# Optimization experiments

Measured on AMD Instinct MI355X. Metric: run time of the kernel, lower is better.

The kernel has to match this reference:

```python
import jax, jax.numpy as jnp
import numpy as np
from jax import lax

V, E, T, F, K = 100000, 300, 50, 100, 3
B, S = 32, 512


def setup_inputs() -> dict:
    key = jax.random.key(0)
    ks = jax.random.split(key, 10)
    inp = {
        "x": jax.random.randint(ks[0], (B, S), 0, V),
        "tags": jax.random.randint(ks[1], (B, S), 0, T),
        "emb": jax.random.normal(ks[2], (V, E), dtype=jnp.float32),
        "conv_w": jax.random.normal(ks[3], (F, E, K), dtype=jnp.float32) / np.sqrt(E * K),
        "conv_b": jnp.zeros((F,), dtype=jnp.float32),
        "fc_w": jax.random.normal(ks[4], (T, F), dtype=jnp.float32) / np.sqrt(F),
        "fc_b": jnp.zeros((T,), dtype=jnp.float32),
        "start_trans": jax.random.uniform(ks[5], (T,), dtype=jnp.float32, minval=-0.1, maxval=0.1),
        "end_trans": jax.random.uniform(ks[6], (T,), dtype=jnp.float32, minval=-0.1, maxval=0.1),
        "trans": jax.random.uniform(ks[7], (T, T), dtype=jnp.float32, minval=-0.1, maxval=0.1),
    }
    return inp


def _emissions(x, emb, conv_w, conv_b, fc_w, fc_b):
    e = emb[x]                                   # [B,S,E] embedding gather
    e = jnp.transpose(e, (0, 2, 1))              # [B,E,S]
    h = lax.conv_general_dilated(e, conv_w, (1,), [(K // 2, K // 2)])  # [B,F,S] (NCW/OIW)
    h = jax.nn.relu(h + conv_b[None, :, None])   # dropout is identity in eval
    feat = jnp.transpose(h, (0, 2, 1))           # [B,S,F]
    return (jnp.einsum("bsf,tf->bst", feat, fc_w) + fc_b).astype(jnp.float32)  # [B,S,T]


def _crf_nll(emissions, tags, start_trans, end_trans, trans):
    # numerator: score of the gold tag path (full mask)
    em_tag = jnp.take_along_axis(emissions, tags[..., None], axis=-1)[..., 0]  # [B,S]
    num = (start_trans[tags[:, 0]]
           + em_tag.sum(-1)
           + trans[tags[:, :-1], tags[:, 1:]].sum(-1)
           + end_trans[tags[:, -1]])                                           # [B]

    # denominator: forward algorithm via scan over time
    alpha0 = start_trans[None, :] + emissions[:, 0]                             # [B,T]

    def step(alpha, em_t):
        # alpha: [B,T] prev scores; em_t: [B,T] emissions at t
        new = jax.nn.logsumexp(alpha[:, :, None] + trans[None] + em_t[:, None, :], axis=1)
        return new, None

    alpha, _ = lax.scan(step, alpha0, jnp.transpose(emissions[:, 1:], (1, 0, 2)))
    log_z = jax.nn.logsumexp(alpha + end_trans[None, :], axis=-1)               # [B]
    return -(num - log_z).sum()  # torchcrf default reduction='sum'; model returns -llh


def reference(x, tags, emb, conv_w, conv_b, fc_w, fc_b, start_trans, end_trans, trans):
    emissions = _emissions(x, emb, conv_w, conv_b, fc_w, fc_b)
    return _crf_nll(emissions, tags, start_trans, end_trans, trans)
```

## Files before the change

### kernel.cpp

```cpp
#include <hip/hip_runtime.h>
#include <hip/hip_bf16.h>
#include <math.h>

#define BB 32
#define SS 512
#define EE 300
#define FF 100
#define TT 50
#define CH 16
#define NC 32

typedef __attribute__((ext_vector_type(8))) short v8s;
typedef __attribute__((ext_vector_type(4))) float v4f;
#define MFMA16 __builtin_amdgcn_mfma_f32_16x16x32_bf16

#define AP 328
#define NCH 10
#define CKS 3
#define CHB (128 * 96)
#define A2P 136
#define MP 72

__device__ inline unsigned short f2bf(float v) {
    unsigned u = __float_as_uint(v);
    unsigned r = u + 0x7fff + ((u >> 16) & 1);
    return (unsigned short)(r >> 16);
}
__device__ inline float bf2f(short s) {
    return __uint_as_float(((unsigned)(unsigned short)s) << 16);
}
__device__ inline unsigned pkbf2(float a, float b) {
    __hip_bfloat162 h = __float22bfloat162_rn(make_float2(a, b));
    return *(unsigned*)&h;
}
__device__ inline v8s ldsld8(const short* p) {
    return *(const v8s*)__builtin_assume_aligned(p, 16);
}
__device__ inline void g2lds16(const void* g, void* l) {
    __builtin_amdgcn_global_load_lds(
        (const __attribute__((address_space(1))) unsigned int*)g,
        (__attribute__((address_space(3))) unsigned int*)l, 16, 0, 0);
}

__global__ void prep_kernel(const float* __restrict__ tr, const float* __restrict__ cw,
                            const float* __restrict__ fcw,
                            unsigned short* __restrict__ wB2,
                            unsigned short* __restrict__ fcwT2,
                            unsigned short* __restrict__ AT,
                            unsigned short* __restrict__ Ab,
                            float* __restrict__ accum, unsigned* __restrict__ cnt)
{
    const int gid = blockIdx.x * 256 + threadIdx.x;
    const int gs  = 64 * 256;
    if (gid == 0) { *accum = 0.f; *cnt = 0u; }
    for (int idx = gid; idx < NCH * CKS * 8 * 512; idx += gs) {
        int e = idx & 7, p = (idx >> 3) & 63, blk = idx >> 9;
        int ch = blk / 24, rem = blk - ch * 24;
        int sl = rem >> 3, ft = rem & 7;
        int col = p >> 2, q = p & 3;
        int n  = ft * 16 + col;
        int gk = ch * 96 + sl * 32 + q * 8 + e;
        int kk = gk / 320, ee = gk - kk * 320;
        float v = (n < FF && ee < EE) ? cw[n * 900 + ee * 3 + kk] : 0.f;
        wB2[idx] = f2bf(v);
    }
    for (int idx = gid; idx < 16 * 512; idx += gs) {
        int e = idx & 7, p = (idx >> 3) & 63, blk = idx >> 9;
        int ks = blk >> 2, nt = blk & 3;
        int col = p >> 2, q = p & 3;
        int t = nt * 16 + col, f = ks * 32 + q * 8 + e;
        float v = (t < TT && f < FF) ? fcw[t * FF + f] : 0.f;
        fcwT2[idx] = f2bf(v);
    }
    for (int idx = gid; idx < 64 * 64; idx += gs) {
        int r = idx >> 6, c2 = idx & 63;
        AT[idx] = (r < TT && c2 < TT) ? f2bf(__expf(tr[c2 * TT + r])) : 0;
        Ab[idx] = (r < TT && c2 < TT) ? f2bf(__expf(tr[r * TT + c2])) : 0;
    }
}

__global__ __launch_bounds__(256, 2) void emis_kernel(
    const int* __restrict__ x, const float* __restrict__ emb,
    const unsigned short* __restrict__ wB2, const float* __restrict__ cb,
    const unsigned short* __restrict__ fcwT2, const float* __restrict__ fcb,
    const int* __restrict__ tags,
    float* __restrict__ expem, float* __restrict__ rmv, float* __restrict__ emtag)
{
    __shared__ __align__(16) short ldsA[34 * AP];
    __shared__ __align__(16) short ldsB[2 * CHB];

    const int b    = blockIdx.y;
    const int s0   = blockIdx.x * 32;
    const int tid  = threadIdx.x;
    const int wv   = tid >> 6;
    const int lane = tid & 63;
    const int col  = lane & 15;
    const int q    = lane >> 4;
    const int bofs = ((col << 2) | q) << 3;

#pragma unroll
    for (int it = 0; it < 6; ++it) {
        int seg = it * 4 + wv;
        g2lds16((const char*)wB2 + seg * 1024 + lane * 16,
                (char*)ldsB + seg * 1024);
    }

    int   xr[10], ofs[10], e0a[10];
#pragma unroll
    for (int it = 0; it < 10; ++it) {
        int g = tid + it * 256;
        int r = g / 75, eg = g - r * 75;
        int e0 = eg * 4;
        int src = s0 - 1 + r;
        bool v = (g < 2550) && (src >= 0) && (src < SS);
        xr[it]  = v ? x[b * SS + src] : -1;
        ofs[it] = r * AP + e0;
        e0a[it] = e0;
    }
    float4 vv[10];
#pragma unroll
    for (int it = 0; it < 10; ++it)
        vv[it] = (xr[it] >= 0)
               ? *(const float4*)(emb + (size_t)xr[it] * EE + e0a[it])
               : make_float4(0.f, 0.f, 0.f, 0.f);
#pragma unroll
    for (int it = 0; it < 10; ++it) {
        int g = tid + it * 256;
        if (g < 2550) {
            unsigned lo = pkbf2(vv[it].x, vv[it].y);
            unsigned hi = pkbf2(vv[it].z, vv[it].w);
            *(uint2*)&ldsA[ofs[it]] = make_uint2(lo, hi);
        }
    }
    if (tid < 34 * 5) {
        int r = tid / 5, c0 = 300 + (tid % 5) * 4;
        *(short4*)&ldsA[r * AP + c0] = make_short4(0, 0, 0, 0);
    }

    v4f acc[2][2];
#pragma unroll
    for (int a = 0; a < 2; ++a)
#pragma unroll
        for (int f = 0; f < 2; ++f) acc[a][f] = (v4f){0.f, 0.f, 0.f, 0.f};

    const int ftA = wv * 2, ftB = wv * 2 + 1;
    for (int ch = 0; ch < NCH; ++ch) {
        __syncthreads();
        if (ch < NCH - 1) {
            const char* g = (const char*)(wB2 + (size_t)(ch + 1) * CHB);
            char* l = (char*)ldsB + ((ch + 1) & 1) * (CHB * 2);
#pragma unroll
            for (int it = 0; it < 6; ++it) {
                int seg = it * 4 + wv;
                g2lds16(g + seg * 1024 + lane * 16, l + seg * 1024);
            }
        } else {
#pragma unroll
            for (int it = 0; it < 4; ++it) {
                int seg = it * 4 + wv;
                g2lds16((const char*)fcwT2 + seg * 1024 + lane * 16,
                        (char*)ldsB + seg * 1024);
            }
        }
        const short* Bc = ldsB + (ch & 1) * CHB;
#pragma unroll
        for (int sl = 0; sl < CKS; ++sl) {
            int gk = ch * 96 + sl * 32;
            int kk = (gk >= 640) ? 2 : (gk >= 320 ? 1 : 0);
            int e0 = gk - kk * 320;
            v8s a0 = ldsld8(&ldsA[(col + kk) * AP + e0 + q * 8]);
            v8s a1 = ldsld8(&ldsA[(16 + col + kk) * AP + e0 + q * 8]);
            v8s b0 = ldsld8(&Bc[((sl * 8 + ftA) << 9) + bofs]);
            v8s b1 = ldsld8(&Bc[((sl * 8 + ftB) << 9) + bofs]);
            acc[0][0] = MFMA16(a0, b0, acc[0][0], 0, 0, 0);
            acc[0][1] = MFMA16(a0, b1, acc[0][1], 0, 0, 0);
            acc[1][0] = MFMA16(a1, b0, acc[1][0], 0, 0, 0);
            acc[1][1] = MFMA16(a1, b1, acc[1][1], 0, 0, 0);
        }
    }
    __syncthreads();

    short* A2 = ldsA;
    short* B2 = ldsB;
#pragma unroll
    for (int st = 0; st < 2; ++st)
#pragma unroll
        for (int fi = 0; fi < 2; ++fi) {
            int f = (wv * 2 + fi) * 16 + col;
            float bias = (f < FF) ? cb[f] : 0.f;
#pragma unroll
            for (int rg = 0; rg < 4; ++rg) {
                int s = st * 16 + q * 4 + rg;
                float v = (f < FF) ? fmaxf(acc[st][fi][rg] + bias, 0.f) : 0.f;
                A2[s * A2P + f] = (short)f2bf(v);
            }
        }
    __syncthreads();

    if (wv < 2) {
        v4f a2[4];
#pragma unroll
        for (int nt = 0; nt < 4; ++nt) a2[nt] = (v4f){0.f, 0.f, 0.f, 0.f};
#pragma unroll
        for (int ks = 0; ks < 4; ++ks) {
            v8s af = ldsld8(&A2[(wv * 16 + col) * A2P + ks * 32 + q * 8]);
#pragma unroll
            for (int nt = 0; nt < 4; ++nt) {
                v8s bt = ldsld8(&B2[((ks * 4 + nt) << 9) + bofs]);
                a2[nt] = MFMA16(af, bt, a2[nt], 0, 0, 0);
            }
        }
        float fb0 = fcb[col], fb1 = fcb[16 + col], fb2 = fcb[32 + col];
        float fb3 = (col < 2) ? fcb[48 + col] : 0.f;
#pragma unroll
        for (int rg = 0; rg < 4; ++rg) {
            int s = s0 + wv * 16 + q * 4 + rg;
            float e0v = a2[0][rg] + fb0;
            float e1v = a2[1][rg] + fb1;
            float e2v = a2[2][rg] + fb2;
            float e3v = (col < 2) ? a2[3][rg] + fb3 : -1e30f;
            float m = fmaxf(fmaxf(e0v, e1v), fmaxf(e2v, e3v));
#pragma unroll
            for (int off = 1; off < 16; off <<= 1) m = fmaxf(m, __shfl_xor(m, off));
            int gidx = b * SS + s;
            if (col == 0) rmv[gidx] = m;
            int tg = tags[gidx];
            float* orow = expem + (size_t)gidx * TT;
            orow[col]      = __expf(e0v - m);
            orow[16 + col] = __expf(e1v - m);
            orow[32 + col] = __expf(e2v - m);
            if (col < 2) orow[48 + col] = __expf(e3v - m);
            if (tg == col)            emtag[gidx] = e0v;
            else if (tg == 16 + col)  emtag[gidx] = e1v;
            else if (tg == 32 + col)  emtag[gidx] = e2v;
            else if (col < 2 && tg == 48 + col) emtag[gidx] = e3v;
        }
    }
}

__global__ __launch_bounds__(64) void chunk_kernel(
    const float* __restrict__ expem, const unsigned short* __restrict__ AT,
    const unsigned short* __restrict__ Ab,
    unsigned short* __restrict__ R, float* __restrict__ lsR)
{
    __shared__ __align__(16) short L[2][64 * MP];
    __shared__ __align__(16) float emL[CH][64];
    const int c = blockIdx.x, b = blockIdx.y;
    const int lane = threadIdx.x;
    const int col = lane & 15, q = lane >> 4;
    const int t0 = c * CH + 1;
    const int nf = (c == NC - 1) ? (SS - 1 - (NC - 1) * CH) : CH;

    for (int idx = lane; idx < CH * 64; idx += 64) {
        int k = idx >> 6, m = idx & 63;
        float v = 0.f;
        if (m < TT && k < nf) v = expem[((size_t)(b * SS + t0 + k)) * TT + m];
        emL[k][m] = v;
    }

    v8s af[4][2];
#pragma unroll
    for (int jt = 0; jt < 4; ++jt)
#pragma unroll
        for (int kc = 0; kc < 2; ++kc)
            af[jt][kc] = *(const v8s*)(AT + (jt * 16 + col) * 64 + kc * 32 + q * 8);
    __syncthreads();

    {
        const v8s* arow = (const v8s*)(Ab + lane * 64);
#pragma unroll
        for (int g = 0; g < 8; ++g) {
            v8s a = arow[g];
            float f[8];
#pragma unroll
            for (int e = 0; e < 8; ++e) f[e] = bf2f(a[e]) * emL[0][g * 8 + e];
            uint4 o = make_uint4(pkbf2(f[0], f[1]), pkbf2(f[2], f[3]),
                                 pkbf2(f[4], f[5]), pkbf2(f[6], f[7]));
            *(uint4*)&L[0][lane * MP + g * 8] = o;
        }
    }

    int cur = 0;
    for (int k = 1; k < nf; ++k) {
        __syncthreads();
        v8s bf[4][2];
#pragma unroll
        for (int nt = 0; nt < 4; ++nt)
#pragma unroll
            for (int kc = 0; kc < 2; ++kc)
                bf[nt][kc] = ldsld8(&L[cur][(nt * 16 + col) * MP + kc * 32 + q * 8]);
        v4f acc[4][4];
#pragma unroll
        for (int jt = 0; jt < 4; ++jt)
#pragma unroll
            for (int nt = 0; nt < 4; ++nt) {
                acc[jt][nt] = (v4f){0.f, 0.f, 0.f, 0.f};
                acc[jt][nt] = MFMA16(af[jt][0], bf[nt][0], acc[jt][nt], 0, 0, 0);
                acc[jt][nt] = MFMA16(af[jt][1], bf[nt][1], acc[jt][nt], 0, 0, 0);
            }
        if (k < nf - 1) {
#pragma unroll
            for (int jt = 0; jt < 4; ++jt) {
                const float4 em4 = *(const float4*)&emL[k][jt * 16 + q * 4];
#pragma unroll
                for (int nt = 0; nt < 4; ++nt) {
                    uint2 o = make_uint2(
                        pkbf2(acc[jt][nt][0] * em4.x, acc[jt][nt][1] * em4.y),
                        pkbf2(acc[jt][nt][2] * em4.z, acc[jt][nt][3] * em4.w));
                    *(uint2*)&L[cur ^ 1][(nt * 16 + col) * MP + jt * 16 + q * 4] = o;
                }
            }
            cur ^= 1;
        } else {
            float vals[4][4][4];
            float mx = 0.f;
#pragma unroll
            for (int jt = 0; jt < 4; ++jt) {
                const float4 em4 = *(const float4*)&emL[k][jt * 16 + q * 4];
#pragma unroll
                for (int nt = 0; nt < 4; ++nt) {
                    vals[jt][nt][0] = acc[jt][nt][0] * em4.x;
                    vals[jt][nt][1] = acc[jt][nt][1] * em4.y;
                    vals[jt][nt][2] = acc[jt][nt][2] * em4.z;
                    vals[jt][nt][3] = acc[jt][nt][3] * em4.w;
#pragma unroll
                    for (int r = 0; r < 4; ++r) mx = fmaxf(mx, vals[jt][nt][r]);
                }
            }
#pragma unroll
            for (int off = 1; off < 64; off <<= 1) mx = fmaxf(mx, __shfl_xor(mx, off));
            mx = fmaxf(mx, 1e-37f);
            float inv = 1.f / mx;
            unsigned short* Rc = R + ((size_t)(b * NC + c) << 12);
#pragma unroll
            for (int jt = 0; jt < 4; ++jt)
#pragma unroll
                for (int nt = 0; nt < 4; ++nt)
#pragma unroll
                    for (int r = 0; r < 4; ++r)
                        Rc[(jt * 16 + q * 4 + r) * 64 + nt * 16 + col] =
                            f2bf(vals[jt][nt][r] * inv);
            if (lane == 0) lsR[b * NC + c] = __logf(mx);
        }
    }
}

__device__ inline float chaindot(const v8s (&buf)[8], const float* pvec) {
    const float4* pv4 = (const float4*)__builtin_assume_aligned(pvec, 16);
    float a0 = 0.f, a1 = 0.f, a2 = 0.f, a3 = 0.f;
#pragma unroll
    for (int g = 0; g < 8; ++g) {
        v8s v = buf[g];
        float4 pA = pv4[g * 2], pB = pv4[g * 2 + 1];
        float* aa = (g & 3) == 0 ? &a0 : (g & 3) == 1 ? &a1 : (g & 3) == 2 ? &a2 : &a3;
        float t = *aa;
        t = fmaf(bf2f(v[0]), pA.x, t);
        t = fmaf(bf2f(v[1]), pA.y, t);
        t = fmaf(bf2f(v[2]), pA.z, t);
        t = fmaf(bf2f(v[3]), pA.w, t);
        t = fmaf(bf2f(v[4]), pB.x, t);
        t = fmaf(bf2f(v[5]), pB.y, t);
        t = fmaf(bf2f(v[6]), pB.z, t);
        t = fmaf(bf2f(v[7]), pB.w, t);
        *aa = t;
    }
    return (a0 + a1) + (a2 + a3);
}

__device__ inline void chainfin(float acc2, float* pvec, int i, float& logacc) {
    float mx = acc2;
#pragma unroll
    for (int off = 1; off < 64; off <<= 1) mx = fmaxf(mx, __shfl_xor(mx, off));
    mx = fmaxf(mx, 1e-37f);
    logacc += __logf(mx);
    pvec[i] = acc2 * (1.f / mx);
}

__global__ __launch_bounds__(256) void chain_kernel(
    const float* __restrict__ expem, const unsigned short* __restrict__ R,
    const float* __restrict__ lsR, const float* __restrict__ start,
    const float* __restrict__ endt,
    const float* __restrict__ emtag, const float* __restrict__ rmv,
    const int* __restrict__ tags, const float* __restrict__ tr,
    float* __restrict__ accum, unsigned* __restrict__ cnt,
    float* __restrict__ out)
{
    __shared__ __align__(16) float pvec[64];
    __shared__ float red[8];
    __shared__ float lzsh;
    const int b = blockIdx.x, tid = threadIdx.x;
    const int wv = tid >> 6, i = tid & 63;

    if (wv == 0) {
        pvec[i] = (i < TT) ? __expf(start[i]) * expem[((size_t)(b * SS)) * TT + i] : 0.f;
        float lsv = (i < NC) ? lsR[b * NC + i] : 0.f;
#pragma unroll
        for (int off = 1; off < 64; off <<= 1) lsv += __shfl_xor(lsv, off);

        const unsigned short* Rb = R + ((size_t)(b * NC) << 12);
        v8s bufA[8], bufB[8];
#pragma unroll
        for (int g = 0; g < 8; ++g)
            bufA[g] = *(const v8s*)(Rb + i * 64 + g * 8);
        float logacc = 0.f;
#pragma unroll 1
        for (int cc = 0; cc < NC; cc += 2) {
            const unsigned short* R1 = Rb + ((size_t)(cc + 1) << 12);
#pragma unroll
            for (int g = 0; g < 8; ++g)
                bufB[g] = *(const v8s*)(R1 + i * 64 + g * 8);
            float acc2 = chaindot(bufA, pvec);
            chainfin(acc2, pvec, i, logacc);
            if (cc + 2 < NC) {
                const unsigned short* R2 = Rb + ((size_t)(cc + 2) << 12);
#pragma unroll
                for (int g = 0; g < 8; ++g)
                    bufA[g] = *(const v8s*)(R2 + i * 64 + g * 8);
            }
            acc2 = chaindot(bufB, pvec);
            chainfin(acc2, pvec, i, logacc);
        }
        float sv = (i < TT) ? pvec[i] * __expf(endt[i]) : 0.f;
#pragma unroll
        for (int off = 1; off < 64; off <<= 1) sv += __shfl_xor(sv, off);
        if (i == 0) lzsh = logacc + lsv + __logf(sv);
    } else {
        float accN = 0.f, accR = 0.f;
        for (int s = tid - 64; s < SS; s += 192) {
            int gi = b * SS + s;
            accN += emtag[gi];
            accR += rmv[gi];
            int tg = tags[gi];
            if (s < SS - 1) accN += tr[tg * TT + tags[gi + 1]];
        }
#pragma unroll
        for (int off = 1; off < 64; off <<= 1) {
            accN += __shfl_xor(accN, off);
            accR += __shfl_xor(accR, off);
        }
        if (i == 0) { red[wv] = accN; red[4 + wv] = accR; }
    }
    __syncthreads();
    if (tid == 0) {
        float tn  = red[1] + red[2] + red[3];
        float trm = red[5] + red[6] + red[7];
        float num = tn + start[tags[b * SS]] + endt[tags[b * SS + SS - 1]];
        float nll = trm + lzsh - num;
        atomicAdd(accum, nll);
        __threadfence();
        unsigned old = atomicAdd(cnt, 1u);
        if (old == BB - 1) out[0] = atomicAdd(accum, 0.f);
    }
}

extern "C" void kernel_launch(void* const* d_in, const int* in_sizes, int n_in,
                              void* d_out, int out_size, void* d_ws, size_t ws_size,
                              hipStream_t stream)
{
    const int*   x    = (const int*)d_in[0];
    const int*   tags = (const int*)d_in[1];
    const float* emb  = (const float*)d_in[2];
    const float* cw   = (const float*)d_in[3];
    const float* cb   = (const float*)d_in[4];
    const float* fcw  = (const float*)d_in[5];
    const float* fcb  = (const float*)d_in[6];
    const float* st   = (const float*)d_in[7];
    const float* en   = (const float*)d_in[8];
    const float* tr   = (const float*)d_in[9];

    unsigned short* wB2   = (unsigned short*)d_ws;
    unsigned short* fcwT2 = wB2 + NCH * CKS * 8 * 512;
    unsigned short* ATm   = fcwT2 + 16 * 512;
    unsigned short* Abm   = ATm + 4096;
    unsigned short* Rm    = Abm + 4096;
    float* fbase   = (float*)(Rm + (size_t)BB * NC * 4096);
    float* expem   = fbase;
    float* rmv     = expem + (size_t)BB * SS * TT;
    float* emtag   = rmv + BB * SS;
    float* lsR     = emtag + BB * SS;
    float* accum   = lsR + BB * NC;
    unsigned* cnt  = (unsigned*)(accum + 1);

    prep_kernel<<<dim3(64), 256, 0, stream>>>(tr, cw, fcw, wB2, fcwT2, ATm, Abm,
                                              accum, cnt);
    emis_kernel<<<dim3(16, BB), 256, 0, stream>>>(x, emb, wB2, cb, fcwT2, fcb,
                                                  tags, expem, rmv, emtag);
    chunk_kernel<<<dim3(NC, BB), 64, 0, stream>>>(expem, ATm, Abm, Rm, lsR);
    chain_kernel<<<dim3(BB), 256, 0, stream>>>(expem, Rm, lsR, st, en,
                                               emtag, rmv, tags, tr,
                                               accum, cnt, (float*)d_out);
}
```

Measured before the change: 239.7 us.

## Split chunk transfer-matrix product across two waves and combine halves

The chunk kernel now runs two waves per block. Each wave computes the running product of transfer matrices over half of the 16-step chunk, using a wave-local LDS double buffer and an lgkmcnt wait instead of a block barrier. Wave 0 then multiplies the two half-products, normalises the result and writes it out. The intent is to halve the serial MFMA dependency chain inside each chunk. The cost is an extra 64x64 matrix product, more LDS, and a transposed scalar store path for the second wave.

```diff
diff --git a/kernel.cpp b/kernel.cpp
--- a/kernel.cpp
+++ b/kernel.cpp
@@ -40,6 +40,11 @@
     __builtin_amdgcn_global_load_lds(
         (const __attribute__((address_space(1))) unsigned int*)g,
         (__attribute__((address_space(3))) unsigned int*)l, 16, 0, 0);
+}
+__device__ inline void wavesync() {
+    __builtin_amdgcn_sched_barrier(0);
+    asm volatile("s_waitcnt lgkmcnt(0)" ::: "memory");
+    __builtin_amdgcn_sched_barrier(0);
 }
 
 __global__ void prep_kernel(const float* __restrict__ tr, const float* __restrict__ cw,
@@ -238,20 +243,45 @@
     }
 }
 
-__global__ __launch_bounds__(64) void chunk_kernel(
+__device__ inline void prodLDS(const short* SA, const short* SB, int col, int q,
+                               v4f (&acc)[4][4]) {
+    v8s a[4][2], bb[4][2];
+#pragma unroll
+    for (int jt = 0; jt < 4; ++jt)
+#pragma unroll
+        for (int kc = 0; kc < 2; ++kc)
+            a[jt][kc] = ldsld8(&SA[(jt * 16 + col) * MP + kc * 32 + q * 8]);
+#pragma unroll
+    for (int nt = 0; nt < 4; ++nt)
+#pragma unroll
+        for (int kc = 0; kc < 2; ++kc)
+            bb[nt][kc] = ldsld8(&SB[(nt * 16 + col) * MP + kc * 32 + q * 8]);
+#pragma unroll
+    for (int jt = 0; jt < 4; ++jt)
+#pragma unroll
+        for (int nt = 0; nt < 4; ++nt) {
+            acc[jt][nt] = (v4f){0.f, 0.f, 0.f, 0.f};
+            acc[jt][nt] = MFMA16(a[jt][0], bb[nt][0], acc[jt][nt], 0, 0, 0);
+            acc[jt][nt] = MFMA16(a[jt][1], bb[nt][1], acc[jt][nt], 0, 0, 0);
+        }
+}
+
+__global__ __launch_bounds__(128) void chunk_kernel(
     const float* __restrict__ expem, const unsigned short* __restrict__ AT,
     const unsigned short* __restrict__ Ab,
     unsigned short* __restrict__ R, float* __restrict__ lsR)
 {
-    __shared__ __align__(16) short L[2][64 * MP];
+    __shared__ __align__(16) short L[4][64 * MP];
     __shared__ __align__(16) float emL[CH][64];
     const int c = blockIdx.x, b = blockIdx.y;
-    const int lane = threadIdx.x;
+    const int tid  = threadIdx.x;
+    const int wv   = tid >> 6;
+    const int lane = tid & 63;
     const int col = lane & 15, q = lane >> 4;
     const int t0 = c * CH + 1;
     const int nf = (c == NC - 1) ? (SS - 1 - (NC - 1) * CH) : CH;
 
-    for (int idx = lane; idx < CH * 64; idx += 64) {
+    for (int idx = tid; idx < CH * 64; idx += 128) {
         int k = idx >> 6, m = idx & 63;
         float v = 0.f;
         if (m < TT && k < nf) v = expem[((size_t)(b * SS + t0 + k)) * TT + m];
@@ -266,6 +296,10 @@
             af[jt][kc] = *(const v8s*)(AT + (jt * 16 + col) * 64 + kc * 32 + q * 8);
     __syncthreads();
 
+    const int k0 = wv * 8;
+    const int hn = wv ? (nf - 8) : 8;
+    short* Lp = &L[wv * 2][0];
+
     {
         const v8s* arow = (const v8s*)(Ab + lane * 64);
 #pragma unroll
@@ -273,22 +307,24 @@
             v8s a = arow[g];
             float f[8];
 #pragma unroll
-            for (int e = 0; e < 8; ++e) f[e] = bf2f(a[e]) * emL[0][g * 8 + e];
+            for (int e = 0; e < 8; ++e) f[e] = bf2f(a[e]) * emL[k0][g * 8 + e];
             uint4 o = make_uint4(pkbf2(f[0], f[1]), pkbf2(f[2], f[3]),
                                  pkbf2(f[4], f[5]), pkbf2(f[6], f[7]));
-            *(uint4*)&L[0][lane * MP + g * 8] = o;
+            *(uint4*)&Lp[lane * MP + g * 8] = o;
         }
     }
 
     int cur = 0;
-    for (int k = 1; k < nf; ++k) {
-        __syncthreads();
+    for (int j = 1; j < hn; ++j) {
+        const int k = k0 + j;
+        wavesync();
         v8s bf[4][2];
 #pragma unroll
         for (int nt = 0; nt < 4; ++nt)
 #pragma unroll
             for (int kc = 0; kc < 2; ++kc)
-                bf[nt][kc] = ldsld8(&L[cur][(nt * 16 + col) * MP + kc * 32 + q * 8]);
+                bf[nt][kc] = ldsld8(&Lp[cur * (64 * MP) +
+                                        (nt * 16 + col) * MP + kc * 32 + q * 8]);
         v4f acc[4][4];
 #pragma unroll
         for (int jt = 0; jt < 4; ++jt)
@@ -298,7 +334,8 @@
                 acc[jt][nt] = MFMA16(af[jt][0], bf[nt][0], acc[jt][nt], 0, 0, 0);
                 acc[jt][nt] = MFMA16(af[jt][1], bf[nt][1], acc[jt][nt], 0, 0, 0);
             }
-        if (k < nf - 1) {
+        short* Ld = &Lp[(cur ^ 1) * (64 * MP)];
+        if (j < hn - 1) {
 #pragma unroll
             for (int jt = 0; jt < 4; ++jt) {
                 const float4 em4 = *(const float4*)&emL[k][jt * 16 + q * 4];
@@ -307,42 +344,64 @@
                     uint2 o = make_uint2(
                         pkbf2(acc[jt][nt][0] * em4.x, acc[jt][nt][1] * em4.y),
                         pkbf2(acc[jt][nt][2] * em4.z, acc[jt][nt][3] * em4.w));
-                    *(uint2*)&L[cur ^ 1][(nt * 16 + col) * MP + jt * 16 + q * 4] = o;
+                    *(uint2*)&Ld[(nt * 16 + col) * MP + jt * 16 + q * 4] = o;
                 }
             }
             cur ^= 1;
-        } else {
-            float vals[4][4][4];
-            float mx = 0.f;
+        } else if (wv == 0) {
 #pragma unroll
             for (int jt = 0; jt < 4; ++jt) {
                 const float4 em4 = *(const float4*)&emL[k][jt * 16 + q * 4];
 #pragma unroll
                 for (int nt = 0; nt < 4; ++nt) {
-                    vals[jt][nt][0] = acc[jt][nt][0] * em4.x;
-                    vals[jt][nt][1] = acc[jt][nt][1] * em4.y;
-                    vals[jt][nt][2] = acc[jt][nt][2] * em4.z;
-                    vals[jt][nt][3] = acc[jt][nt][3] * em4.w;
-#pragma unroll
-                    for (int r = 0; r < 4; ++r) mx = fmaxf(mx, vals[jt][nt][r]);
+                    uint2 o = make_uint2(
+                        pkbf2(acc[jt][nt][0] * em4.x, acc[jt][nt][1] * em4.y),
+                        pkbf2(acc[jt][nt][2] * em4.z, acc[jt][nt][3] * em4.w));
+                    *(uint2*)&Ld[(nt * 16 + col) * MP + jt * 16 + q * 4] = o;
                 }
             }
-#pragma unroll
-            for (int off = 1; off < 64; off <<= 1) mx = fmaxf(mx, __shfl_xor(mx, off));
-            mx = fmaxf(mx, 1e-37f);
-            float inv = 1.f / mx;
-            unsigned short* Rc = R + ((size_t)(b * NC + c) << 12);
-#pragma unroll
-            for (int jt = 0; jt < 4; ++jt)
-#pragma unroll
-                for (int nt = 0; nt < 4; ++nt)
-#pragma unroll
-                    for (int r = 0; r < 4; ++r)
-                        Rc[(jt * 16 + q * 4 + r) * 64 + nt * 16 + col] =
-                            f2bf(vals[jt][nt][r] * inv);
-            if (lane == 0) lsR[b * NC + c] = __logf(mx);
-        }
-    }
+        } else {
+#pragma unroll
+            for (int jt = 0; jt < 4; ++jt) {
+                const float4 em4 = *(const float4*)&emL[k][jt * 16 + q * 4];
+#pragma unroll
+                for (int nt = 0; nt < 4; ++nt) {
+                    Ld[(jt * 16 + q * 4 + 0) * MP + nt * 16 + col] = (short)f2bf(acc[jt][nt][0] * em4.x);
+                    Ld[(jt * 16 + q * 4 + 1) * MP + nt * 16 + col] = (short)f2bf(acc[jt][nt][1] * em4.y);
+                    Ld[(jt * 16 + q * 4 + 2) * MP + nt * 16 + col] = (short)f2bf(acc[jt][nt][2] * em4.z);
+                    Ld[(jt * 16 + q * 4 + 3) * MP + nt * 16 + col] = (short)f2bf(acc[jt][nt][3] * em4.w);
+                }
+            }
+        }
+    }
+    __syncthreads();
+    if (wv != 0) return;
+
+    const short* H0 = &L[0][0] + 1 * (64 * MP);
+    const short* H1 = &L[2][0] + (((nf - 8) - 1) & 1) * (64 * MP);
+    v4f acc[4][4];
+    prodLDS(H1, H0, col, q, acc);
+    float mx = 0.f;
+#pragma unroll
+    for (int jt = 0; jt < 4; ++jt)
+#pragma unroll
+        for (int nt = 0; nt < 4; ++nt)
+#pragma unroll
+            for (int r = 0; r < 4; ++r) mx = fmaxf(mx, acc[jt][nt][r]);
+#pragma unroll
+    for (int off = 1; off < 64; off <<= 1) mx = fmaxf(mx, __shfl_xor(mx, off));
+    mx = fmaxf(mx, 1e-37f);
+    float inv = 1.f / mx;
+    unsigned short* Rc = R + ((size_t)(b * NC + c) << 12);
+#pragma unroll
+    for (int jt = 0; jt < 4; ++jt)
+#pragma unroll
+        for (int nt = 0; nt < 4; ++nt)
+#pragma unroll
+            for (int r = 0; r < 4; ++r)
+                Rc[(jt * 16 + q * 4 + r) * 64 + nt * 16 + col] =
+                    f2bf(acc[jt][nt][r] * inv);
+    if (lane == 0) lsR[b * NC + c] = __logf(mx);
 }
 
 __device__ inline float chaindot(const v8s (&buf)[8], const float* pvec) {
@@ -485,7 +544,7 @@
                                               accum, cnt);
     emis_kernel<<<dim3(16, BB), 256, 0, stream>>>(x, emb, wB2, cb, fcwT2, fcb,
                                                   tags, expem, rmv, emtag);
-    chunk_kernel<<<dim3(NC, BB), 64, 0, stream>>>(expem, ATm, Abm, Rm, lsR);
+    chunk_kernel<<<dim3(NC, BB), 128, 0, stream>>>(expem, ATm, Abm, Rm, lsR);
     chain_kernel<<<dim3(BB), 256, 0, stream>>>(expem, Rm, lsR, st, en,
                                                emtag, rmv, tags, tr,
                                                accum, cnt, (float*)d_out);
```

Result: no change. 237.9 us (-0.7%).
